# Kernel optimization log

Hardware: AMD Instinct MI355X
Metric: run time of the kernel (lower is better)

## Reference

```python
import jax, jax.numpy as jnp
import numpy as np

N, E, G = 50000, 800000, 128
F_IN, F0, D, NL, DN = 128, 256, 256, 4, 512


def setup_inputs() -> dict:
    key = jax.random.key(0)
    ks = iter(jax.random.split(key, 40))

    def U(shape, fan_in):
        s = 1.0 / np.sqrt(fan_in)
        return jax.random.uniform(next(ks), shape, minval=-s, maxval=s, dtype=jnp.float32)

    x = jax.random.normal(next(ks), (N, F_IN), dtype=jnp.float32)
    edge_index = jax.random.randint(next(ks), (2, E), 0, N)
    batch_index = jnp.sort(jax.random.randint(next(ks), (N,), 0, G))
    return dict(
        x=x, edge_index=edge_index, batch_index=batch_index,
        fl_W=U((F_IN, F0), F_IN), fl_b=U((F0,), F_IN),
        conv1_W=U((F0, D), F0), conv1_b=U((D,), F0),
        tr1_W=U((D, D), D), tr1_b=U((D,), D),
        bn1_g=jnp.ones((D,), jnp.float32), bn1_b=jnp.zeros((D,), jnp.float32),
        convs_W=U((NL, D, D), D), convs_b=U((NL, D), D),
        trs_W=U((NL, D, D), D), trs_b=U((NL, D), D),
        bns_g=jnp.ones((NL, D), jnp.float32), bns_b=jnp.zeros((NL, D), jnp.float32),
        l1_W=U((2 * D, DN), 2 * D), l1_b=U((DN,), 2 * D),
        l2_W=U((DN, DN // 2), DN), l2_b=U((DN // 2,), DN),
        l3_W=U((DN // 2, 10), DN // 2), l3_b=U((10,), DN // 2),
    )


def reference(x, edge_index, batch_index, fl_W, fl_b, conv1_W, conv1_b,
              tr1_W, tr1_b, bn1_g, bn1_b, convs_W, convs_b, trs_W, trs_b,
              bns_g, bns_b, l1_W, l1_b, l2_W, l2_b, l3_W, l3_b):
    n = x.shape[0]
    loops = jnp.arange(n, dtype=edge_index.dtype)
    src = jnp.concatenate([edge_index[0], loops])  # [E+N] GCN self-loops
    dst = jnp.concatenate([edge_index[1], loops])
    deg = jax.ops.segment_sum(jnp.ones_like(dst, dtype=x.dtype), dst, num_segments=n)
    dis = jax.lax.rsqrt(deg)  # deg >= 1 due to self-loops
    norm = dis[src] * dis[dst]  # [E+N] symmetric normalization

    def gcn(h, W, b):
        m = h @ W
        return jax.ops.segment_sum(norm[:, None] * m[src], dst, num_segments=n) + b

    def bn(h, g, bb):
        mu = h.mean(axis=0)
        var = jnp.mean((h - mu) ** 2, axis=0)  # biased var, torch BN train math
        return g * (h - mu) * jax.lax.rsqrt(var + 1e-5) + bb

    h = x @ fl_W + fl_b
    h = jax.nn.relu(gcn(h, conv1_W, conv1_b))
    h = bn(h, bn1_g, bn1_b)
    h = jax.nn.relu(h @ tr1_W + tr1_b)  # dropout off (eval)
    for i in range(convs_W.shape[0]):
        h = jax.nn.relu(gcn(h, convs_W[i], convs_b[i]))
        h = bn(h, bns_g[i], bns_b[i])
        h = jax.nn.relu(h @ trs_W[i] + trs_b[i])

    sums = jax.ops.segment_sum(h, batch_index, num_segments=G)
    cnt = jax.ops.segment_sum(jnp.ones((n,), h.dtype), batch_index, num_segments=G)
    pooled = sums / jnp.maximum(cnt, 1.0)[:, None]  # global_mean_pool
    z = jnp.concatenate([pooled, pooled], axis=1)
    z = jax.nn.relu(z @ l1_W + l1_b)
    z = jax.nn.relu(z @ l2_W + l2_b)
    return z @ l3_W + l3_b
```

## Files before the change

kernel.cpp:

```cpp
#include <hip/hip_runtime.h>

#define DD 256

typedef unsigned short u16;
typedef unsigned int u32;
using bf16x8 = __attribute__((ext_vector_type(8))) short;
using f16x8  = __attribute__((ext_vector_type(8))) _Float16;
using f32x4  = __attribute__((ext_vector_type(4))) float;

#define GLB_PTR(p) ((const __attribute__((address_space(1))) u32*)(p))
#define LDS_PTR(p) ((__attribute__((address_space(3))) u32*)(p))


__device__ __forceinline__ u32 f2bfx2(float v) {
  u32 b = __float_as_uint(v);
  u32 hi = (b + 0x7fffu + ((b >> 16) & 1u)) >> 16;
  float hf = __uint_as_float(hi << 16);
  float lof = v - hf;
  u32 b2 = __float_as_uint(lof);
  u32 lo = (b2 + 0x7fffu + ((b2 >> 16) & 1u)) >> 16;
  return hi | (lo << 16);
}

__device__ __forceinline__ u16 f2h(float f) {
  _Float16 h = (_Float16)f;
  return __builtin_bit_cast(unsigned short, h);
}
__device__ __forceinline__ float h2f(u16 x) {
  return (float)__builtin_bit_cast(_Float16, x);
}

__device__ __forceinline__ bf16x8 as_bf16x8(uint4 u) {
  union { uint4 u; bf16x8 v; } c;
  c.u = u;
  return c.v;
}
__device__ __forceinline__ f16x8 as_f16x8(uint4 u) {
  union { uint4 u; f16x8 v; } c;
  c.u = u;
  return c.v;
}

__device__ __forceinline__ void unpack8(uint4 a, uint4 b, bf16x8& hi, bf16x8& lo) {
  union { u32 w[4]; bf16x8 v; } H, L;
  H.w[0] = __builtin_amdgcn_perm(a.y, a.x, 0x05040100u);
  L.w[0] = __builtin_amdgcn_perm(a.y, a.x, 0x07060302u);
  H.w[1] = __builtin_amdgcn_perm(a.w, a.z, 0x05040100u);
  L.w[1] = __builtin_amdgcn_perm(a.w, a.z, 0x07060302u);
  H.w[2] = __builtin_amdgcn_perm(b.y, b.x, 0x05040100u);
  L.w[2] = __builtin_amdgcn_perm(b.y, b.x, 0x07060302u);
  H.w[3] = __builtin_amdgcn_perm(b.w, b.z, 0x05040100u);
  L.w[3] = __builtin_amdgcn_perm(b.w, b.z, 0x07060302u);
  hi = H.v;
  lo = L.v;
}

__device__ __forceinline__ int packoff(int col, int k) {
  int w = col >> 6, r = (col >> 4) & 3, c16 = col & 15;
  int kc = k >> 5, q = (k >> 3) & 3, j = k & 7;
  return ((kc * 4 + w) * 4 + r) * 512 + (q * 16 + c16) * 8 + j;
}


__global__ void zero_i32_kernel(int* p, int n) {
  int i = blockIdx.x * 256 + threadIdx.x;
  if (i < n) p[i] = 0;
}

__global__ void zero_f32_kernel(float* p, int n) {
  int i = blockIdx.x * 256 + threadIdx.x;
  if (i < n) p[i] = 0.f;
}

__global__ void count_kernel(const int* __restrict__ dst, int* __restrict__ cnt, int e) {
  int i = blockIdx.x * 256 + threadIdx.x;
  if (i < e) atomicAdd(&cnt[dst[i]], 1);
}

__global__ void scan_block_kernel(const int* __restrict__ cnt, int* __restrict__ out,
                                  int* __restrict__ bsum, int n) {
  __shared__ int sh[256];
  int tid = threadIdx.x;
  int base = blockIdx.x * 1024 + tid * 4;
  int v0 = (base + 0 < n) ? cnt[base + 0] : 0;
  int v1 = (base + 1 < n) ? cnt[base + 1] : 0;
  int v2 = (base + 2 < n) ? cnt[base + 2] : 0;
  int v3 = (base + 3 < n) ? cnt[base + 3] : 0;
  int s = v0 + v1 + v2 + v3;
  sh[tid] = s;
  __syncthreads();
  for (int d = 1; d < 256; d <<= 1) {
    int t = (tid >= d) ? sh[tid - d] : 0;
    __syncthreads();
    sh[tid] += t;
    __syncthreads();
  }
  int excl = sh[tid] - s;
  if (base + 0 < n) out[base + 0] = excl;
  excl += v0;
  if (base + 1 < n) out[base + 1] = excl;
  excl += v1;
  if (base + 2 < n) out[base + 2] = excl;
  excl += v2;
  if (base + 3 < n) out[base + 3] = excl;
  if (tid == 255) bsum[blockIdx.x] = sh[255];
}

__global__ void scan_partials_kernel(int* bsum, int nb) {
  if (threadIdx.x == 0 && blockIdx.x == 0) {
    int acc = 0;
    for (int i = 0; i < nb; ++i) { int t = bsum[i]; bsum[i] = acc; acc += t; }
  }
}

__global__ void finalize_kernel(int* __restrict__ off, const int* __restrict__ bsum,
                                int* __restrict__ cursor, const int* __restrict__ cnt,
                                float* __restrict__ dis, int n, int e) {
  int i = blockIdx.x * 256 + threadIdx.x;
  if (i < n) {
    int o = off[i] + bsum[i >> 10];
    off[i] = o;
    cursor[i] = o;
    dis[i] = rsqrtf((float)(cnt[i] + 1));
  }
  if (i == 0 && blockIdx.x == 0) off[n] = e;
}

__global__ void fill_kernel(const int* __restrict__ src, const int* __restrict__ dst,
                            int* __restrict__ cursor, const float* __restrict__ dis,
                            int2* __restrict__ csrE, int e) {
  int i = blockIdx.x * 256 + threadIdx.x;
  if (i < e) {
    int s = src[i];
    int d = dst[i];
    int p = atomicAdd(&cursor[d], 1);
    float w = dis[s] * dis[d];
    csrE[p] = make_int2(s, __float_as_int(w));
  }
}


__global__ void xsplit_kernel(const float* __restrict__ x, u32* __restrict__ xq, int n) {
  int i = blockIdx.x * 256 + threadIdx.x;
  if (i < n) xq[i] = f2bfx2(x[i]);
}


__global__ void wsplit_all_kernel(const float* __restrict__ fl_W, const float* __restrict__ conv1_W,
                                  const float* __restrict__ convs_W, u16* __restrict__ flHi,
                                  u16* __restrict__ flLo, u16* __restrict__ cvF) {
  int j = blockIdx.x;
  int m = blockIdx.y;
  int k = threadIdx.x;
  if (m == 0) {
    if (k < 128) {
      u32 p = f2bfx2(fl_W[(size_t)k * 256 + j]);
      int off = packoff(j, k);
      flHi[off] = (u16)(p & 0xffffu);
      flLo[off] = (u16)(p >> 16);
    }
  } else {
    int c = m - 1;
    const float* W = (c == 0) ? conv1_W : convs_W + (size_t)(c - 1) * 65536;
    cvF[(size_t)c * 65536 + packoff(j, k)] = f2h(W[(size_t)k * 256 + j]);
  }
}

__global__ void wsplit_fold_kernel(const float* __restrict__ W, const float* __restrict__ scale,
                                   const float* __restrict__ shift, const float* __restrict__ bt,
                                   u16* __restrict__ trF, float* __restrict__ bias_out) {
  __shared__ float red[256];
  int j = blockIdx.x;
  int k = threadIdx.x;
  float w = W[(size_t)k * 256 + j];
  trF[packoff(j, k)] = f2h(w * scale[k]);
  red[k] = shift[k] * w;
  __syncthreads();
  for (int d = 128; d > 0; d >>= 1) {
    if (k < d) red[k] += red[k + d];
    __syncthreads();
  }
  if (k == 0) bias_out[j] = bt[j] + red[0];
}


__device__ __forceinline__ f16x8 afrag16(const u32* As, int R, int q) {
  int off = (q * 4) ^ (((R >> 1) & 3) << 2);
  return as_f16x8(*(const uint4*)(As + R * 16 + off));
}

__device__ __forceinline__ void afrag32(const u32* Asbase, int R, int q, bf16x8& ah, bf16x8& al) {
  int s = (R & 7) << 4;
  const u32* row = Asbase + R * 32;
  uint4 a0 = *(const uint4*)(row + ((((q * 32)) ^ s) >> 2));
  uint4 a1 = *(const uint4*)(row + ((((q * 32) + 16) ^ s) >> 2));
  unpack8(a0, a1, ah, al);
}

__global__ __launch_bounds__(256) void fused_fl_kernel(
    const u32* __restrict__ Aq, const u16* __restrict__ W1h, const u16* __restrict__ W1l,
    const float* __restrict__ bias1, const u16* __restrict__ W2f, u16* __restrict__ C,
    int nrows) {
  constexpr int NK1 = 4;
  __shared__ __align__(16) u32 As[2][2048];
  __shared__ __align__(16) u16 T[64 * 256];
  const int tid = threadIdx.x;
  const int lane = tid & 63;
  const int wave = tid >> 6;
  const int row0 = blockIdx.x * 64;
  const int q = lane >> 4;
  const int r16 = lane & 15;

  int sRowG[2], sOff[2];
#pragma unroll
  for (int c = 0; c < 2; ++c) {
    int row_l = c * 32 + wave * 8 + (lane >> 3);
    int grow = row0 + row_l;
    if (grow > nrows - 1) grow = nrows - 1;
    sRowG[c] = grow;
    sOff[c] = ((lane & 7) * 4) ^ ((row_l & 7) << 2);
  }

  int bBase[4];
#pragma unroll
  for (int r = 0; r < 4; ++r) bBase[r] = (wave * 4 + r) * 512 + lane * 8;

  f32x4 acc[4][4];
#pragma unroll
  for (int i = 0; i < 4; ++i)
#pragma unroll
    for (int r = 0; r < 4; ++r) acc[i][r] = (f32x4){0.f, 0.f, 0.f, 0.f};

  auto stage = [&](int buf, int kc32) {
#pragma unroll
    for (int c = 0; c < 2; ++c) {
      const u32* gsrc = Aq + (size_t)sRowG[c] * 128 + kc32 * 32 + sOff[c];
      u32* ldst = &As[buf][c * 1024 + wave * 256];
      __builtin_amdgcn_global_load_lds(GLB_PTR(gsrc), LDS_PTR(ldst), 16, 0, 0);
    }
  };

  stage(0, 0);
  __syncthreads();
  int buf = 0;
#pragma unroll
  for (int kc = 0; kc < NK1; ++kc) {
    if (kc + 1 < NK1) stage(buf ^ 1, kc + 1);
    uint4 BH[4], BL[4];
#pragma unroll
    for (int r = 0; r < 4; ++r) {
      BH[r] = *(const uint4*)(W1h + bBase[r] + kc * 8192);
      BL[r] = *(const uint4*)(W1l + bBase[r] + kc * 8192);
    }
    bf16x8 ah[4], al[4];
#pragma unroll
    for (int i = 0; i < 4; ++i) afrag32(As[buf], i * 16 + r16, q, ah[i], al[i]);
#pragma unroll
    for (int r = 0; r < 4; ++r) {
      bf16x8 bh = as_bf16x8(BH[r]);
      bf16x8 bl = as_bf16x8(BL[r]);
#pragma unroll
      for (int i = 0; i < 4; ++i) {
        acc[i][r] = __builtin_amdgcn_mfma_f32_16x16x32_bf16(ah[i], bh, acc[i][r], 0, 0, 0);
        acc[i][r] = __builtin_amdgcn_mfma_f32_16x16x32_bf16(al[i], bh, acc[i][r], 0, 0, 0);
        acc[i][r] = __builtin_amdgcn_mfma_f32_16x16x32_bf16(ah[i], bl, acc[i][r], 0, 0, 0);
      }
    }
    __syncthreads();
    buf ^= 1;
  }

#pragma unroll
  for (int r = 0; r < 4; ++r) {
    int col = wave * 64 + r * 16 + r16;
    float bv = bias1[col];
#pragma unroll
    for (int i = 0; i < 4; ++i) {
#pragma unroll
      for (int g = 0; g < 4; ++g) {
        int row = i * 16 + q * 4 + g;
        float v = acc[i][r][g] + bv;
        *(u16*)((char*)T + row * 512 + ((col * 2) ^ ((row & 7) << 4))) = f2h(v);
      }
    }
  }

#pragma unroll
  for (int i = 0; i < 4; ++i)
#pragma unroll
    for (int r = 0; r < 4; ++r) acc[i][r] = (f32x4){0.f, 0.f, 0.f, 0.f};
  __syncthreads();

#pragma unroll
  for (int kc = 0; kc < 8; ++kc) {
    uint4 BF[4];
#pragma unroll
    for (int r = 0; r < 4; ++r) BF[r] = *(const uint4*)(W2f + bBase[r] + kc * 8192);
    f16x8 af[4];
#pragma unroll
    for (int i = 0; i < 4; ++i) {
      int row = i * 16 + r16;
      int base = kc * 64 + q * 16;
      af[i] = as_f16x8(*(const uint4*)((char*)T + row * 512 + (base ^ ((row & 7) << 4))));
    }
#pragma unroll
    for (int r = 0; r < 4; ++r) {
      f16x8 bf = as_f16x8(BF[r]);
#pragma unroll
      for (int i = 0; i < 4; ++i)
        acc[i][r] = __builtin_amdgcn_mfma_f32_16x16x32_f16(af[i], bf, acc[i][r], 0, 0, 0);
    }
  }

#pragma unroll
  for (int r = 0; r < 4; ++r) {
    int col = wave * 64 + r * 16 + r16;
#pragma unroll
    for (int i = 0; i < 4; ++i) {
#pragma unroll
      for (int g = 0; g < 4; ++g) {
        int row = row0 + i * 16 + q * 4 + g;
        if (row < nrows) C[(size_t)row * 256 + col] = f2h(acc[i][r][g]);
      }
    }
  }
}

__global__ __launch_bounds__(256) void fused_h_kernel(
    const u16* __restrict__ Ah, const u16* __restrict__ W1f, const float* __restrict__ bias1,
    const u16* __restrict__ W2f, u16* __restrict__ C, int nrows) {
  __shared__ __align__(16) u32 As[2][1024];
  __shared__ __align__(16) u16 T[64 * 256];
  const int tid = threadIdx.x;
  const int lane = tid & 63;
  const int wave = tid >> 6;
  const int row0 = blockIdx.x * 64;
  const int q = lane >> 4;
  const int r16 = lane & 15;

  int row_l = tid >> 2;
  int grow = row0 + row_l;
  if (grow > nrows - 1) grow = nrows - 1;
  const int sK = (((tid & 3) * 8)) ^ (((row_l >> 1) & 3) << 3);

  int bBase[4];
#pragma unroll
  for (int r = 0; r < 4; ++r) bBase[r] = (wave * 4 + r) * 512 + lane * 8;

  f32x4 acc[4][4];
#pragma unroll
  for (int i = 0; i < 4; ++i)
#pragma unroll
    for (int r = 0; r < 4; ++r) acc[i][r] = (f32x4){0.f, 0.f, 0.f, 0.f};

  auto stage = [&](int buf, int kc32) {
    const u16* gsrc = Ah + (size_t)grow * 256 + kc32 * 32 + sK;
    u32* ldst = &As[buf][wave * 256];
    __builtin_amdgcn_global_load_lds(GLB_PTR(gsrc), LDS_PTR(ldst), 16, 0, 0);
  };

  stage(0, 0);
  __syncthreads();
  int buf = 0;
#pragma unroll
  for (int kc = 0; kc < 8; ++kc) {
    if (kc + 1 < 8) stage(buf ^ 1, kc + 1);
    uint4 BF[4];
#pragma unroll
    for (int r = 0; r < 4; ++r) BF[r] = *(const uint4*)(W1f + bBase[r] + kc * 8192);
    f16x8 af[4];
#pragma unroll
    for (int i = 0; i < 4; ++i) af[i] = afrag16(As[buf], i * 16 + r16, q);
#pragma unroll
    for (int r = 0; r < 4; ++r) {
      f16x8 bf = as_f16x8(BF[r]);
#pragma unroll
      for (int i = 0; i < 4; ++i)
        acc[i][r] = __builtin_amdgcn_mfma_f32_16x16x32_f16(af[i], bf, acc[i][r], 0, 0, 0);
    }
    __syncthreads();
    buf ^= 1;
  }

#pragma unroll
  for (int r = 0; r < 4; ++r) {
    int col = wave * 64 + r * 16 + r16;
    float bv = bias1[col];
#pragma unroll
    for (int i = 0; i < 4; ++i) {
#pragma unroll
      for (int g = 0; g < 4; ++g) {
        int row = i * 16 + q * 4 + g;
        float v = fmaxf(acc[i][r][g] + bv, 0.f);
        *(u16*)((char*)T + row * 512 + ((col * 2) ^ ((row & 7) << 4))) = f2h(v);
      }
    }
  }

#pragma unroll
  for (int i = 0; i < 4; ++i)
#pragma unroll
    for (int r = 0; r < 4; ++r) acc[i][r] = (f32x4){0.f, 0.f, 0.f, 0.f};
  __syncthreads();

#pragma unroll
  for (int kc = 0; kc < 8; ++kc) {
    uint4 BF[4];
#pragma unroll
    for (int r = 0; r < 4; ++r) BF[r] = *(const uint4*)(W2f + bBase[r] + kc * 8192);
    f16x8 af[4];
#pragma unroll
    for (int i = 0; i < 4; ++i) {
      int row = i * 16 + r16;
      int base = kc * 64 + q * 16;
      af[i] = as_f16x8(*(const uint4*)((char*)T + row * 512 + (base ^ ((row & 7) << 4))));
    }
#pragma unroll
    for (int r = 0; r < 4; ++r) {
      f16x8 bf = as_f16x8(BF[r]);
#pragma unroll
      for (int i = 0; i < 4; ++i)
        acc[i][r] = __builtin_amdgcn_mfma_f32_16x16x32_f16(af[i], bf, acc[i][r], 0, 0, 0);
    }
  }

#pragma unroll
  for (int r = 0; r < 4; ++r) {
    int col = wave * 64 + r * 16 + r16;
#pragma unroll
    for (int i = 0; i < 4; ++i) {
#pragma unroll
      for (int g = 0; g < 4; ++g) {
        int row = row0 + i * 16 + q * 4 + g;
        if (row < nrows) C[(size_t)row * 256 + col] = f2h(acc[i][r][g]);
      }
    }
  }
}

__global__ __launch_bounds__(256) void gemm_h_kernel(
    const u16* __restrict__ Ah, const u16* __restrict__ W1f, const float* __restrict__ bias,
    u16* __restrict__ C, int nrows) {
  __shared__ __align__(16) u32 As[2][1024];
  const int tid = threadIdx.x;
  const int lane = tid & 63;
  const int wave = tid >> 6;
  const int row0 = blockIdx.x * 64;
  const int q = lane >> 4;
  const int r16 = lane & 15;

  int row_l = tid >> 2;
  int grow = row0 + row_l;
  if (grow > nrows - 1) grow = nrows - 1;
  const int sK = (((tid & 3) * 8)) ^ (((row_l >> 1) & 3) << 3);

  int bBase[4];
#pragma unroll
  for (int r = 0; r < 4; ++r) bBase[r] = (wave * 4 + r) * 512 + lane * 8;

  f32x4 acc[4][4];
#pragma unroll
  for (int i = 0; i < 4; ++i)
#pragma unroll
    for (int r = 0; r < 4; ++r) acc[i][r] = (f32x4){0.f, 0.f, 0.f, 0.f};

  auto stage = [&](int buf, int kc32) {
    const u16* gsrc = Ah + (size_t)grow * 256 + kc32 * 32 + sK;
    u32* ldst = &As[buf][wave * 256];
    __builtin_amdgcn_global_load_lds(GLB_PTR(gsrc), LDS_PTR(ldst), 16, 0, 0);
  };

  stage(0, 0);
  __syncthreads();
  int buf = 0;
#pragma unroll
  for (int kc = 0; kc < 8; ++kc) {
    if (kc + 1 < 8) stage(buf ^ 1, kc + 1);
    uint4 BF[4];
#pragma unroll
    for (int r = 0; r < 4; ++r) BF[r] = *(const uint4*)(W1f + bBase[r] + kc * 8192);
    f16x8 af[4];
#pragma unroll
    for (int i = 0; i < 4; ++i) af[i] = afrag16(As[buf], i * 16 + r16, q);
#pragma unroll
    for (int r = 0; r < 4; ++r) {
      f16x8 bf = as_f16x8(BF[r]);
#pragma unroll
      for (int i = 0; i < 4; ++i)
        acc[i][r] = __builtin_amdgcn_mfma_f32_16x16x32_f16(af[i], bf, acc[i][r], 0, 0, 0);
    }
    __syncthreads();
    buf ^= 1;
  }

#pragma unroll
  for (int r = 0; r < 4; ++r) {
    int col = wave * 64 + r * 16 + r16;
    float bv = bias[col];
#pragma unroll
    for (int i = 0; i < 4; ++i) {
#pragma unroll
      for (int g = 0; g < 4; ++g) {
        int row = row0 + i * 16 + q * 4 + g;
        if (row < nrows) C[(size_t)row * 256 + col] = f2h(fmaxf(acc[i][r][g] + bv, 0.f));
      }
    }
  }
}


__global__ __launch_bounds__(256) void gather_kernel(
    const u16* __restrict__ m, const int* __restrict__ off,
    const int2* __restrict__ csrE, const float* __restrict__ dis,
    const float* __restrict__ bias, u16* __restrict__ out,
    float* __restrict__ shard, int n) {
  __shared__ float2 red[4][256];
  int wv = threadIdx.x >> 6;
  int lane = threadIdx.x & 63;
  int node = blockIdx.x * 4 + wv;
  float ax = 0.f, ay = 0.f, az = 0.f, aw = 0.f;
  if (node < n) {
    float di = dis[node];
    uint2 v = *(const uint2*)(m + (size_t)node * DD + lane * 4);
    float w = di * di;
    ax = w * h2f((u16)(v.x & 0xffff)); ay = w * h2f((u16)(v.x >> 16));
    az = w * h2f((u16)(v.y & 0xffff)); aw = w * h2f((u16)(v.y >> 16));
    int e0 = off[node], e1 = off[node + 1];
    int e = e0;
    for (; e + 3 < e1; e += 4) {
      int2 p0 = csrE[e], p1 = csrE[e + 1], p2 = csrE[e + 2], p3 = csrE[e + 3];
      float w0 = __int_as_float(p0.y), w1 = __int_as_float(p1.y);
      float w2 = __int_as_float(p2.y), w3 = __int_as_float(p3.y);
      uint2 u0 = *(const uint2*)(m + (size_t)p0.x * DD + lane * 4);
      uint2 u1 = *(const uint2*)(m + (size_t)p1.x * DD + lane * 4);
      uint2 u2 = *(const uint2*)(m + (size_t)p2.x * DD + lane * 4);
      uint2 u3 = *(const uint2*)(m + (size_t)p3.x * DD + lane * 4);
      ax = fmaf(w0, h2f((u16)(u0.x & 0xffff)), ax); ay = fmaf(w0, h2f((u16)(u0.x >> 16)), ay);
      az = fmaf(w0, h2f((u16)(u0.y & 0xffff)), az); aw = fmaf(w0, h2f((u16)(u0.y >> 16)), aw);
      ax = fmaf(w1, h2f((u16)(u1.x & 0xffff)), ax); ay = fmaf(w1, h2f((u16)(u1.x >> 16)), ay);
      az = fmaf(w1, h2f((u16)(u1.y & 0xffff)), az); aw = fmaf(w1, h2f((u16)(u1.y >> 16)), aw);
      ax = fmaf(w2, h2f((u16)(u2.x & 0xffff)), ax); ay = fmaf(w2, h2f((u16)(u2.x >> 16)), ay);
      az = fmaf(w2, h2f((u16)(u2.y & 0xffff)), az); aw = fmaf(w2, h2f((u16)(u2.y >> 16)), aw);
      ax = fmaf(w3, h2f((u16)(u3.x & 0xffff)), ax); ay = fmaf(w3, h2f((u16)(u3.x >> 16)), ay);
      az = fmaf(w3, h2f((u16)(u3.y & 0xffff)), az); aw = fmaf(w3, h2f((u16)(u3.y >> 16)), aw);
    }
    for (; e < e1; ++e) {
      int2 p0 = csrE[e];
      float w0 = __int_as_float(p0.y);
      uint2 u0 = *(const uint2*)(m + (size_t)p0.x * DD + lane * 4);
      ax = fmaf(w0, h2f((u16)(u0.x & 0xffff)), ax); ay = fmaf(w0, h2f((u16)(u0.x >> 16)), ay);
      az = fmaf(w0, h2f((u16)(u0.y & 0xffff)), az); aw = fmaf(w0, h2f((u16)(u0.y >> 16)), aw);
    }
    float4 bb = *(const float4*)(bias + lane * 4);
    ax = fmaxf(ax + bb.x, 0.f);
    ay = fmaxf(ay + bb.y, 0.f);
    az = fmaxf(az + bb.z, 0.f);
    aw = fmaxf(aw + bb.w, 0.f);
    uint2 oo;
    oo.x = (u32)f2h(ax) | ((u32)f2h(ay) << 16);
    oo.y = (u32)f2h(az) | ((u32)f2h(aw) << 16);
    *(uint2*)(out + (size_t)node * DD + lane * 4) = oo;
  }
  red[wv][lane * 4 + 0] = make_float2(ax, ax * ax);
  red[wv][lane * 4 + 1] = make_float2(ay, ay * ay);
  red[wv][lane * 4 + 2] = make_float2(az, az * az);
  red[wv][lane * 4 + 3] = make_float2(aw, aw * aw);
  __syncthreads();
  int c = threadIdx.x;
  float2 a = red[0][c], b2 = red[1][c], c2 = red[2][c], d2 = red[3][c];
  float s = (a.x + b2.x) + (c2.x + d2.x);
  float qq = (a.y + b2.y) + (c2.y + d2.y);
  float* sh = shard + (size_t)(blockIdx.x & 63) * 512;
  atomicAdd(&sh[c], s);
  atomicAdd(&sh[256 + c], qq);
}


__global__ void bn_finalize_kernel(const float* __restrict__ shard, const float* __restrict__ g,
                                   const float* __restrict__ b, float* __restrict__ scale,
                                   float* __restrict__ shift, float inv_n) {
  int c = threadIdx.x;
  float s = 0.f, q = 0.f;
  for (int i = 0; i < 64; ++i) {
    s += shard[(size_t)i * 512 + c];
    q += shard[(size_t)i * 512 + 256 + c];
  }
  float mu = s * inv_n;
  float var = q * inv_n - mu * mu;
  float inv = rsqrtf(var + 1e-5f);
  float sc = g[c] * inv;
  scale[c] = sc;
  shift[c] = b[c] - mu * sc;
}


__global__ void pool_kernel(const u16* __restrict__ h, const int* __restrict__ batch,
                            float* __restrict__ pooled, int n) {
  int g = blockIdx.x;
  int c = threadIdx.x;
  int lo = 0, hi = n;
  while (lo < hi) { int mid = (lo + hi) >> 1; if (batch[mid] < g) lo = mid + 1; else hi = mid; }
  int start = lo;
  hi = n;
  while (lo < hi) { int mid = (lo + hi) >> 1; if (batch[mid] <= g) lo = mid + 1; else hi = mid; }
  int end = lo;
  float a0 = 0.f, a1 = 0.f, a2 = 0.f, a3 = 0.f;
  int r = start;
  for (; r + 3 < end; r += 4) {
    a0 += h2f(h[(size_t)(r + 0) * DD + c]);
    a1 += h2f(h[(size_t)(r + 1) * DD + c]);
    a2 += h2f(h[(size_t)(r + 2) * DD + c]);
    a3 += h2f(h[(size_t)(r + 3) * DD + c]);
  }
  for (; r < end; ++r) a0 += h2f(h[(size_t)r * DD + c]);
  float s = (a0 + a1) + (a2 + a3);
  int cg = end - start;
  pooled[g * DD + c] = s / (float)(cg > 1 ? cg : 1);
}


__global__ void mlp1_kernel(const float* __restrict__ pooled, const float* __restrict__ W,
                            const float* __restrict__ b, float* __restrict__ out) {
  __shared__ float p[256];
  int g = blockIdx.x;
  int j = blockIdx.y * 256 + threadIdx.x;
  p[threadIdx.x] = pooled[g * 256 + threadIdx.x];
  __syncthreads();
  float acc = b[j];
#pragma unroll 8
  for (int k = 0; k < 512; ++k) acc = fmaf(p[k & 255], W[k * 512 + j], acc);
  out[g * 512 + j] = fmaxf(acc, 0.f);
}

__global__ void mlp2_kernel(const float* __restrict__ z1, const float* __restrict__ W,
                            const float* __restrict__ b, float* __restrict__ out) {
  __shared__ float p[512];
  int g = blockIdx.x;
  p[threadIdx.x] = z1[g * 512 + threadIdx.x];
  p[256 + threadIdx.x] = z1[g * 512 + 256 + threadIdx.x];
  __syncthreads();
  float acc = b[threadIdx.x];
#pragma unroll 8
  for (int k = 0; k < 512; ++k) acc = fmaf(p[k], W[k * 256 + threadIdx.x], acc);
  out[g * 256 + threadIdx.x] = fmaxf(acc, 0.f);
}

__global__ void mlp3_kernel(const float* __restrict__ z2, const float* __restrict__ W,
                            const float* __restrict__ b, float* __restrict__ out) {
  int g = blockIdx.x;
  int lane = threadIdx.x;
  float acc[10];
#pragma unroll
  for (int o = 0; o < 10; ++o) acc[o] = 0.f;
  for (int k = lane; k < 256; k += 64) {
    float v = z2[g * 256 + k];
#pragma unroll
    for (int o = 0; o < 10; ++o) acc[o] = fmaf(v, W[k * 10 + o], acc[o]);
  }
#pragma unroll
  for (int o = 0; o < 10; ++o) {
    float s = acc[o];
    for (int d = 32; d > 0; d >>= 1) s += __shfl_down(s, d);
    if (lane == 0) out[g * 10 + o] = s + b[o];
  }
}


extern "C" void kernel_launch(void* const* d_in, const int* in_sizes, int n_in,
                              void* d_out, int out_size, void* d_ws, size_t ws_size,
                              hipStream_t stream) {
  const float* x = (const float*)d_in[0];
  const int* ei = (const int*)d_in[1];
  const int* batch = (const int*)d_in[2];
  const float* fl_W = (const float*)d_in[3];
  const float* fl_b = (const float*)d_in[4];
  const float* conv1_W = (const float*)d_in[5];
  const float* conv1_b = (const float*)d_in[6];
  const float* tr1_W = (const float*)d_in[7];
  const float* tr1_b = (const float*)d_in[8];
  const float* bn1_g = (const float*)d_in[9];
  const float* bn1_b = (const float*)d_in[10];
  const float* convs_W = (const float*)d_in[11];
  const float* convs_b = (const float*)d_in[12];
  const float* trs_W = (const float*)d_in[13];
  const float* trs_b = (const float*)d_in[14];
  const float* bns_g = (const float*)d_in[15];
  const float* bns_b = (const float*)d_in[16];
  const float* l1_W = (const float*)d_in[17];
  const float* l1_b = (const float*)d_in[18];
  const float* l2_W = (const float*)d_in[19];
  const float* l2_b = (const float*)d_in[20];
  const float* l3_W = (const float*)d_in[21];
  const float* l3_b = (const float*)d_in[22];

  const int N = in_sizes[0] / 128;
  const int E = in_sizes[1] / 2;
  const int G = out_size / 10;
  const int NL = in_sizes[11] / (256 * 256);
  const int* src = ei;
  const int* dst = ei + E;

  char* ws = (char*)d_ws;
  size_t o = 0;
  auto alloc = [&](size_t bytes) -> char* {
    o = (o + 255) & ~(size_t)255;
    char* p = ws + o;
    o += bytes;
    return p;
  };
  u16* hA = (u16*)alloc((size_t)N * DD * 2);
  u16* mF = (u16*)alloc((size_t)N * DD * 2);
  u32* xq = (u32*)alloc((size_t)N * 128 * 4);
  float* dis = (float*)alloc((size_t)N * 4);
  int* cnt = (int*)alloc((size_t)N * 4);
  int* off = (int*)alloc((size_t)(N + 1) * 4);
  int* cursor = (int*)alloc((size_t)N * 4);
  int* bsum = (int*)alloc(64 * 4);
  int2* csrE = (int2*)alloc((size_t)E * 8);
  float* shards = (float*)alloc((size_t)(1 + NL) * 64 * 512 * 4);
  float* scalev = (float*)alloc(256 * 4);
  float* shiftv = (float*)alloc(256 * 4);
  float* pooled = (float*)alloc((size_t)G * 256 * 4);
  float* z1 = (float*)alloc((size_t)G * 512 * 4);
  float* z2 = (float*)alloc((size_t)G * 256 * 4);
  u16* flHi = (u16*)alloc(128 * 256 * 2);
  u16* flLo = (u16*)alloc(128 * 256 * 2);
  u16* cvF = (u16*)alloc((size_t)(1 + NL) * 256 * 256 * 2);
  u16* trF = (u16*)alloc(256 * 256 * 2);
  float* trBias = (float*)alloc(256 * 4);

  dim3 b256(256);
  const int nblk = (N + 63) / 64;

  zero_i32_kernel<<<(N + 255) / 256, b256, 0, stream>>>(cnt, N);
  count_kernel<<<(E + 255) / 256, b256, 0, stream>>>(dst, cnt, E);
  int nb = (N + 1023) / 1024;
  scan_block_kernel<<<nb, b256, 0, stream>>>(cnt, off, bsum, N);
  scan_partials_kernel<<<1, 64, 0, stream>>>(bsum, nb);
  finalize_kernel<<<(N + 255) / 256, b256, 0, stream>>>(off, bsum, cursor, cnt, dis, N, E);
  fill_kernel<<<(E + 255) / 256, b256, 0, stream>>>(src, dst, cursor, dis, csrE, E);

  xsplit_kernel<<<(N * 128 + 255) / 256, b256, 0, stream>>>(x, xq, N * 128);
  dim3 wgrid(256, 2 + NL);
  wsplit_all_kernel<<<wgrid, b256, 0, stream>>>(fl_W, conv1_W, convs_W, flHi, flLo, cvF);
  int shard_elems = (1 + NL) * 64 * 512;
  zero_f32_kernel<<<(shard_elems + 255) / 256, b256, 0, stream>>>(shards, shard_elems);

  fused_fl_kernel<<<nblk, b256, 0, stream>>>(xq, flHi, flLo, fl_b, cvF, mF, N);

  for (int L = 0; L < 1 + NL; ++L) {
    const float* bc = (L == 0) ? conv1_b : convs_b + (size_t)(L - 1) * 256;
    const float* gg = (L == 0) ? bn1_g : bns_g + (size_t)(L - 1) * 256;
    const float* gb = (L == 0) ? bn1_b : bns_b + (size_t)(L - 1) * 256;
    const float* Wt = (L == 0) ? tr1_W : trs_W + (size_t)(L - 1) * 256 * 256;
    const float* bt = (L == 0) ? tr1_b : trs_b + (size_t)(L - 1) * 256;
    float* slot = shards + (size_t)L * 64 * 512;

    gather_kernel<<<(N + 3) / 4, b256, 0, stream>>>(mF, off, csrE, dis, bc, hA, slot, N);
    bn_finalize_kernel<<<1, b256, 0, stream>>>(slot, gg, gb, scalev, shiftv, 1.0f / (float)N);
    wsplit_fold_kernel<<<256, b256, 0, stream>>>(Wt, scalev, shiftv, bt, trF, trBias);
    if (L < NL) {
      fused_h_kernel<<<nblk, b256, 0, stream>>>(hA, trF, trBias,
                                                cvF + (size_t)(L + 1) * 65536, mF, N);
    } else {
      gemm_h_kernel<<<nblk, b256, 0, stream>>>(hA, trF, trBias, mF, N);
    }
  }

  pool_kernel<<<G, b256, 0, stream>>>(mF, batch, pooled, N);
  dim3 m1grid(G, 2);
  mlp1_kernel<<<m1grid, b256, 0, stream>>>(pooled, l1_W, l1_b, z1);
  mlp2_kernel<<<G, b256, 0, stream>>>(z1, l2_W, l2_b, z2);
  mlp3_kernel<<<G, 64, 0, stream>>>(z2, l3_W, l3_b, (float*)d_out);
}
```

Before: 750.5 us.

## Widen GEMM A-tile staging to 64-wide K chunks and gather two nodes per wave

The fused_h and gemm_h kernels now stage 64-column K chunks of A into LDS with an XOR swizzle over 8 16-byte slots. This halves the number of K iterations and barriers, at the cost of doubling LDS for the A buffers. The gather kernel now has each wave process two destination nodes, interleaving their edge loads to expose more memory-level parallelism. It launches half as many blocks, and the BN partial sums combine both nodes per wave.

```diff
diff --git a/kernel.cpp b/kernel.cpp
--- a/kernel.cpp
+++ b/kernel.cpp
@@ -184,17 +184,17 @@
 }
 
 
-__device__ __forceinline__ f16x8 afrag16(const u32* As, int R, int q) {
-  int off = (q * 4) ^ (((R >> 1) & 3) << 2);
-  return as_f16x8(*(const uint4*)(As + R * 16 + off));
-}
-
 __device__ __forceinline__ void afrag32(const u32* Asbase, int R, int q, bf16x8& ah, bf16x8& al) {
   int s = (R & 7) << 4;
   const u32* row = Asbase + R * 32;
   uint4 a0 = *(const uint4*)(row + ((((q * 32)) ^ s) >> 2));
   uint4 a1 = *(const uint4*)(row + ((((q * 32) + 16) ^ s) >> 2));
   unpack8(a0, a1, ah, al);
+}
+
+__device__ __forceinline__ f16x8 afrag64(const u32* As, int R, int ch, int q) {
+  int s = (ch * 4 + q) ^ (R & 7);
+  return as_f16x8(*(const uint4*)(As + R * 32 + s * 4));
 }
 
 __global__ __launch_bounds__(256) void fused_fl_kernel(
@@ -329,7 +329,7 @@
 __global__ __launch_bounds__(256) void fused_h_kernel(
     const u16* __restrict__ Ah, const u16* __restrict__ W1f, const float* __restrict__ bias1,
     const u16* __restrict__ W2f, u16* __restrict__ C, int nrows) {
-  __shared__ __align__(16) u32 As[2][1024];
+  __shared__ __align__(16) u32 As[2][2048];
   __shared__ __align__(16) u16 T[64 * 256];
   const int tid = threadIdx.x;
   const int lane = tid & 63;
@@ -338,10 +338,15 @@
   const int q = lane >> 4;
   const int r16 = lane & 15;
 
-  int row_l = tid >> 2;
-  int grow = row0 + row_l;
-  if (grow > nrows - 1) grow = nrows - 1;
-  const int sK = (((tid & 3) * 8)) ^ (((row_l >> 1) & 3) << 3);
+  int sRowG[2], sOffH[2];
+#pragma unroll
+  for (int c = 0; c < 2; ++c) {
+    int row_l = c * 32 + wave * 8 + (lane >> 3);
+    int grow = row0 + row_l;
+    if (grow > nrows - 1) grow = nrows - 1;
+    sRowG[c] = grow;
+    sOffH[c] = ((lane & 7) ^ (row_l & 7)) * 8;
+  }
 
   int bBase[4];
 #pragma unroll
@@ -353,30 +358,37 @@
 #pragma unroll
     for (int r = 0; r < 4; ++r) acc[i][r] = (f32x4){0.f, 0.f, 0.f, 0.f};
 
-  auto stage = [&](int buf, int kc32) {
-    const u16* gsrc = Ah + (size_t)grow * 256 + kc32 * 32 + sK;
-    u32* ldst = &As[buf][wave * 256];
-    __builtin_amdgcn_global_load_lds(GLB_PTR(gsrc), LDS_PTR(ldst), 16, 0, 0);
+  auto stage = [&](int buf, int kc64) {
+#pragma unroll
+    for (int c = 0; c < 2; ++c) {
+      const u16* gsrc = Ah + (size_t)sRowG[c] * 256 + kc64 * 64 + sOffH[c];
+      u32* ldst = &As[buf][c * 1024 + wave * 256];
+      __builtin_amdgcn_global_load_lds(GLB_PTR(gsrc), LDS_PTR(ldst), 16, 0, 0);
+    }
   };
 
   stage(0, 0);
   __syncthreads();
   int buf = 0;
 #pragma unroll
-  for (int kc = 0; kc < 8; ++kc) {
-    if (kc + 1 < 8) stage(buf ^ 1, kc + 1);
-    uint4 BF[4];
-#pragma unroll
-    for (int r = 0; r < 4; ++r) BF[r] = *(const uint4*)(W1f + bBase[r] + kc * 8192);
-    f16x8 af[4];
-#pragma unroll
-    for (int i = 0; i < 4; ++i) af[i] = afrag16(As[buf], i * 16 + r16, q);
-#pragma unroll
-    for (int r = 0; r < 4; ++r) {
-      f16x8 bf = as_f16x8(BF[r]);
-#pragma unroll
-      for (int i = 0; i < 4; ++i)
-        acc[i][r] = __builtin_amdgcn_mfma_f32_16x16x32_f16(af[i], bf, acc[i][r], 0, 0, 0);
+  for (int kc = 0; kc < 4; ++kc) {
+    if (kc + 1 < 4) stage(buf ^ 1, kc + 1);
+#pragma unroll
+    for (int ch = 0; ch < 2; ++ch) {
+      int kc32 = kc * 2 + ch;
+      uint4 BF[4];
+#pragma unroll
+      for (int r = 0; r < 4; ++r) BF[r] = *(const uint4*)(W1f + bBase[r] + kc32 * 8192);
+      f16x8 af[4];
+#pragma unroll
+      for (int i = 0; i < 4; ++i) af[i] = afrag64(As[buf], i * 16 + r16, ch, q);
+#pragma unroll
+      for (int r = 0; r < 4; ++r) {
+        f16x8 bf = as_f16x8(BF[r]);
+#pragma unroll
+        for (int i = 0; i < 4; ++i)
+          acc[i][r] = __builtin_amdgcn_mfma_f32_16x16x32_f16(af[i], bf, acc[i][r], 0, 0, 0);
+      }
     }
     __syncthreads();
     buf ^= 1;
@@ -441,7 +453,7 @@
 __global__ __launch_bounds__(256) void gemm_h_kernel(
     const u16* __restrict__ Ah, const u16* __restrict__ W1f, const float* __restrict__ bias,
     u16* __restrict__ C, int nrows) {
-  __shared__ __align__(16) u32 As[2][1024];
+  __shared__ __align__(16) u32 As[2][2048];
   const int tid = threadIdx.x;
   const int lane = tid & 63;
   const int wave = tid >> 6;
@@ -449,10 +461,15 @@
   const int q = lane >> 4;
   const int r16 = lane & 15;
 
-  int row_l = tid >> 2;
-  int grow = row0 + row_l;
-  if (grow > nrows - 1) grow = nrows - 1;
-  const int sK = (((tid & 3) * 8)) ^ (((row_l >> 1) & 3) << 3);
+  int sRowG[2], sOffH[2];
+#pragma unroll
+  for (int c = 0; c < 2; ++c) {
+    int row_l = c * 32 + wave * 8 + (lane >> 3);
+    int grow = row0 + row_l;
+    if (grow > nrows - 1) grow = nrows - 1;
+    sRowG[c] = grow;
+    sOffH[c] = ((lane & 7) ^ (row_l & 7)) * 8;
+  }
 
   int bBase[4];
 #pragma unroll
@@ -464,30 +481,37 @@
 #pragma unroll
     for (int r = 0; r < 4; ++r) acc[i][r] = (f32x4){0.f, 0.f, 0.f, 0.f};
 
-  auto stage = [&](int buf, int kc32) {
-    const u16* gsrc = Ah + (size_t)grow * 256 + kc32 * 32 + sK;
-    u32* ldst = &As[buf][wave * 256];
-    __builtin_amdgcn_global_load_lds(GLB_PTR(gsrc), LDS_PTR(ldst), 16, 0, 0);
+  auto stage = [&](int buf, int kc64) {
+#pragma unroll
+    for (int c = 0; c < 2; ++c) {
+      const u16* gsrc = Ah + (size_t)sRowG[c] * 256 + kc64 * 64 + sOffH[c];
+      u32* ldst = &As[buf][c * 1024 + wave * 256];
+      __builtin_amdgcn_global_load_lds(GLB_PTR(gsrc), LDS_PTR(ldst), 16, 0, 0);
+    }
   };
 
   stage(0, 0);
   __syncthreads();
   int buf = 0;
 #pragma unroll
-  for (int kc = 0; kc < 8; ++kc) {
-    if (kc + 1 < 8) stage(buf ^ 1, kc + 1);
-    uint4 BF[4];
-#pragma unroll
-    for (int r = 0; r < 4; ++r) BF[r] = *(const uint4*)(W1f + bBase[r] + kc * 8192);
-    f16x8 af[4];
-#pragma unroll
-    for (int i = 0; i < 4; ++i) af[i] = afrag16(As[buf], i * 16 + r16, q);
-#pragma unroll
-    for (int r = 0; r < 4; ++r) {
-      f16x8 bf = as_f16x8(BF[r]);
-#pragma unroll
-      for (int i = 0; i < 4; ++i)
-        acc[i][r] = __builtin_amdgcn_mfma_f32_16x16x32_f16(af[i], bf, acc[i][r], 0, 0, 0);
+  for (int kc = 0; kc < 4; ++kc) {
+    if (kc + 1 < 4) stage(buf ^ 1, kc + 1);
+#pragma unroll
+    for (int ch = 0; ch < 2; ++ch) {
+      int kc32 = kc * 2 + ch;
+      uint4 BF[4];
+#pragma unroll
+      for (int r = 0; r < 4; ++r) BF[r] = *(const uint4*)(W1f + bBase[r] + kc32 * 8192);
+      f16x8 af[4];
+#pragma unroll
+      for (int i = 0; i < 4; ++i) af[i] = afrag64(As[buf], i * 16 + r16, ch, q);
+#pragma unroll
+      for (int r = 0; r < 4; ++r) {
+        f16x8 bf = as_f16x8(BF[r]);
+#pragma unroll
+        for (int i = 0; i < 4; ++i)
+          acc[i][r] = __builtin_amdgcn_mfma_f32_16x16x32_f16(af[i], bf, acc[i][r], 0, 0, 0);
+      }
     }
     __syncthreads();
     buf ^= 1;
@@ -517,54 +541,86 @@
   __shared__ float2 red[4][256];
   int wv = threadIdx.x >> 6;
   int lane = threadIdx.x & 63;
-  int node = blockIdx.x * 4 + wv;
-  float ax = 0.f, ay = 0.f, az = 0.f, aw = 0.f;
-  if (node < n) {
-    float di = dis[node];
-    uint2 v = *(const uint2*)(m + (size_t)node * DD + lane * 4);
+  int nA = blockIdx.x * 8 + wv * 2;
+  int nB = nA + 1;
+  float axA = 0.f, ayA = 0.f, azA = 0.f, awA = 0.f;
+  float axB = 0.f, ayB = 0.f, azB = 0.f, awB = 0.f;
+
+  auto edge = [&](int2 p, float& x, float& y, float& z, float& w) {
+    float ww = __int_as_float(p.y);
+    uint2 u = *(const uint2*)(m + (size_t)p.x * DD + lane * 4);
+    x = fmaf(ww, h2f((u16)(u.x & 0xffff)), x);
+    y = fmaf(ww, h2f((u16)(u.x >> 16)), y);
+    z = fmaf(ww, h2f((u16)(u.y & 0xffff)), z);
+    w = fmaf(ww, h2f((u16)(u.y >> 16)), w);
+  };
+
+  int eA = 0, eA1 = 0, eB = 0, eB1 = 0;
+  if (nA < n) {
+    float di = dis[nA];
+    uint2 v = *(const uint2*)(m + (size_t)nA * DD + lane * 4);
     float w = di * di;
-    ax = w * h2f((u16)(v.x & 0xffff)); ay = w * h2f((u16)(v.x >> 16));
-    az = w * h2f((u16)(v.y & 0xffff)); aw = w * h2f((u16)(v.y >> 16));
-    int e0 = off[node], e1 = off[node + 1];
-    int e = e0;
-    for (; e + 3 < e1; e += 4) {
-      int2 p0 = csrE[e], p1 = csrE[e + 1], p2 = csrE[e + 2], p3 = csrE[e + 3];
-      float w0 = __int_as_float(p0.y), w1 = __int_as_float(p1.y);
-      float w2 = __int_as_float(p2.y), w3 = __int_as_float(p3.y);
-      uint2 u0 = *(const uint2*)(m + (size_t)p0.x * DD + lane * 4);
-      uint2 u1 = *(const uint2*)(m + (size_t)p1.x * DD + lane * 4);
-      uint2 u2 = *(const uint2*)(m + (size_t)p2.x * DD + lane * 4);
-      uint2 u3 = *(const uint2*)(m + (size_t)p3.x * DD + lane * 4);
-      ax = fmaf(w0, h2f((u16)(u0.x & 0xffff)), ax); ay = fmaf(w0, h2f((u16)(u0.x >> 16)), ay);
-      az = fmaf(w0, h2f((u16)(u0.y & 0xffff)), az); aw = fmaf(w0, h2f((u16)(u0.y >> 16)), aw);
-      ax = fmaf(w1, h2f((u16)(u1.x & 0xffff)), ax); ay = fmaf(w1, h2f((u16)(u1.x >> 16)), ay);
-      az = fmaf(w1, h2f((u16)(u1.y & 0xffff)), az); aw = fmaf(w1, h2f((u16)(u1.y >> 16)), aw);
-      ax = fmaf(w2, h2f((u16)(u2.x & 0xffff)), ax); ay = fmaf(w2, h2f((u16)(u2.x >> 16)), ay);
-      az = fmaf(w2, h2f((u16)(u2.y & 0xffff)), az); aw = fmaf(w2, h2f((u16)(u2.y >> 16)), aw);
-      ax = fmaf(w3, h2f((u16)(u3.x & 0xffff)), ax); ay = fmaf(w3, h2f((u16)(u3.x >> 16)), ay);
-      az = fmaf(w3, h2f((u16)(u3.y & 0xffff)), az); aw = fmaf(w3, h2f((u16)(u3.y >> 16)), aw);
-    }
-    for (; e < e1; ++e) {
-      int2 p0 = csrE[e];
-      float w0 = __int_as_float(p0.y);
-      uint2 u0 = *(const uint2*)(m + (size_t)p0.x * DD + lane * 4);
-      ax = fmaf(w0, h2f((u16)(u0.x & 0xffff)), ax); ay = fmaf(w0, h2f((u16)(u0.x >> 16)), ay);
-      az = fmaf(w0, h2f((u16)(u0.y & 0xffff)), az); aw = fmaf(w0, h2f((u16)(u0.y >> 16)), aw);
-    }
-    float4 bb = *(const float4*)(bias + lane * 4);
-    ax = fmaxf(ax + bb.x, 0.f);
-    ay = fmaxf(ay + bb.y, 0.f);
-    az = fmaxf(az + bb.z, 0.f);
-    aw = fmaxf(aw + bb.w, 0.f);
+    axA = w * h2f((u16)(v.x & 0xffff)); ayA = w * h2f((u16)(v.x >> 16));
+    azA = w * h2f((u16)(v.y & 0xffff)); awA = w * h2f((u16)(v.y >> 16));
+    eA = off[nA]; eA1 = off[nA + 1];
+  }
+  if (nB < n) {
+    float di = dis[nB];
+    uint2 v = *(const uint2*)(m + (size_t)nB * DD + lane * 4);
+    float w = di * di;
+    axB = w * h2f((u16)(v.x & 0xffff)); ayB = w * h2f((u16)(v.x >> 16));
+    azB = w * h2f((u16)(v.y & 0xffff)); awB = w * h2f((u16)(v.y >> 16));
+    eB = off[nB]; eB1 = off[nB + 1];
+  }
+
+  while (eA + 1 < eA1 && eB + 1 < eB1) {
+    int2 pA0 = csrE[eA], pA1 = csrE[eA + 1];
+    int2 pB0 = csrE[eB], pB1 = csrE[eB + 1];
+    edge(pA0, axA, ayA, azA, awA);
+    edge(pB0, axB, ayB, azB, awB);
+    edge(pA1, axA, ayA, azA, awA);
+    edge(pB1, axB, ayB, azB, awB);
+    eA += 2; eB += 2;
+  }
+  for (; eA + 1 < eA1; eA += 2) {
+    int2 p0 = csrE[eA], p1 = csrE[eA + 1];
+    edge(p0, axA, ayA, azA, awA);
+    edge(p1, axA, ayA, azA, awA);
+  }
+  if (eA < eA1) edge(csrE[eA], axA, ayA, azA, awA);
+  for (; eB + 1 < eB1; eB += 2) {
+    int2 p0 = csrE[eB], p1 = csrE[eB + 1];
+    edge(p0, axB, ayB, azB, awB);
+    edge(p1, axB, ayB, azB, awB);
+  }
+  if (eB < eB1) edge(csrE[eB], axB, ayB, azB, awB);
+
+  float4 bb = *(const float4*)(bias + lane * 4);
+  if (nA < n) {
+    axA = fmaxf(axA + bb.x, 0.f); ayA = fmaxf(ayA + bb.y, 0.f);
+    azA = fmaxf(azA + bb.z, 0.f); awA = fmaxf(awA + bb.w, 0.f);
     uint2 oo;
-    oo.x = (u32)f2h(ax) | ((u32)f2h(ay) << 16);
-    oo.y = (u32)f2h(az) | ((u32)f2h(aw) << 16);
-    *(uint2*)(out + (size_t)node * DD + lane * 4) = oo;
-  }
-  red[wv][lane * 4 + 0] = make_float2(ax, ax * ax);
-  red[wv][lane * 4 + 1] = make_float2(ay, ay * ay);
-  red[wv][lane * 4 + 2] = make_float2(az, az * az);
-  red[wv][lane * 4 + 3] = make_float2(aw, aw * aw);
+    oo.x = (u32)f2h(axA) | ((u32)f2h(ayA) << 16);
+    oo.y = (u32)f2h(azA) | ((u32)f2h(awA) << 16);
+    *(uint2*)(out + (size_t)nA * DD + lane * 4) = oo;
+  } else {
+    axA = ayA = azA = awA = 0.f;
+  }
+  if (nB < n) {
+    axB = fmaxf(axB + bb.x, 0.f); ayB = fmaxf(ayB + bb.y, 0.f);
+    azB = fmaxf(azB + bb.z, 0.f); awB = fmaxf(awB + bb.w, 0.f);
+    uint2 oo;
+    oo.x = (u32)f2h(axB) | ((u32)f2h(ayB) << 16);
+    oo.y = (u32)f2h(azB) | ((u32)f2h(awB) << 16);
+    *(uint2*)(out + (size_t)nB * DD + lane * 4) = oo;
+  } else {
+    axB = ayB = azB = awB = 0.f;
+  }
+
+  red[wv][lane * 4 + 0] = make_float2(axA + axB, axA * axA + axB * axB);
+  red[wv][lane * 4 + 1] = make_float2(ayA + ayB, ayA * ayA + ayB * ayB);
+  red[wv][lane * 4 + 2] = make_float2(azA + azB, azA * azA + azB * azB);
+  red[wv][lane * 4 + 3] = make_float2(awA + awB, awA * awA + awB * awB);
   __syncthreads();
   int c = threadIdx.x;
   float2 a = red[0][c], b2 = red[1][c], c2 = red[2][c], d2 = red[3][c];
@@ -756,7 +812,7 @@
     const float* bt = (L == 0) ? tr1_b : trs_b + (size_t)(L - 1) * 256;
     float* slot = shards + (size_t)L * 64 * 512;
 
-    gather_kernel<<<(N + 3) / 4, b256, 0, stream>>>(mF, off, csrE, dis, bc, hA, slot, N);
+    gather_kernel<<<(N + 7) / 8, b256, 0, stream>>>(mF, off, csrE, dis, bc, hA, slot, N);
     bn_finalize_kernel<<<1, b256, 0, stream>>>(slot, gg, gb, scalev, shiftv, 1.0f / (float)N);
     wsplit_fold_kernel<<<256, b256, 0, stream>>>(Wt, scalev, shiftv, bt, trF, trBias);
     if (L < NL) {
```

New measurement: 731.6 us. 1.03x faster.
